# Performance work log

Hardware: AMD Instinct MI355X
Metric: run time of the kernel (lower is better)

Reference implementation:

```python
import jax, jax.numpy as jnp
import numpy as np

M_MARGIN = 0.25
GAMMA = 256.0
NEG_INF = jnp.float32(-1e30)


def setup_inputs() -> dict:
    key = jax.random.key(0)
    k1, k2 = jax.random.split(key)
    feature = jax.random.normal(k1, (8192, 128), dtype=jnp.float32)
    label = jax.random.randint(k2, (8192,), 0, 64, dtype=jnp.int64)
    return {"feature": feature, "label": label}


def reference(feature, label):
    # F.normalize: L2-normalize rows (eps=1e-12)
    norm = jnp.maximum(jnp.linalg.norm(feature, axis=1, keepdims=True), 1e-12)
    f = feature / norm
    sim = f @ f.T  # [N, N]
    N = sim.shape[0]

    same = label[:, None] == label[None, :]
    triu = jnp.triu(jnp.ones((N, N), dtype=bool), k=1)
    pos_mask = same & triu
    neg_mask = (~same) & triu

    sim_d = jax.lax.stop_gradient(sim)  # .detach() in original
    ap = jnp.maximum(-sim_d + 1.0 + M_MARGIN, 0.0)
    an = jnp.maximum(sim_d + M_MARGIN, 0.0)
    delta_p = 1.0 - M_MARGIN
    delta_n = M_MARGIN

    logit_p = -ap * (sim - delta_p) * GAMMA
    logit_n = an * (sim - delta_n) * GAMMA

    # boolean-gather + logsumexp == masked logsumexp (fixed shapes, jit-friendly)
    lse_p = jax.nn.logsumexp(jnp.where(pos_mask, logit_p, NEG_INF))
    lse_n = jax.nn.logsumexp(jnp.where(neg_mask, logit_n, NEG_INF))

    return jax.nn.softplus(lse_n + lse_p)
```

## Files before the change

### kernel.cpp

```cpp
#include <hip/hip_runtime.h>
#include <hip/hip_bf16.h>
#include <math.h>

#define NROW 8192
#define DIM  128
#define BM   64
#define BN   128
#define TM   (NROW / BM)
#define TN   (NROW / BN)
#define NTILES 4160

typedef __bf16 bf16x8 __attribute__((ext_vector_type(8)));
typedef float  f32x4  __attribute__((ext_vector_type(4)));

#define G2      369.3299304675746f
#define NEGBIG  (-3.0e38f)
#define NOFF    2000.0f

__global__ __launch_bounds__(256)
void prep_kernel(const float* __restrict__ f, __hip_bfloat16* __restrict__ fhi) {
    int row  = blockIdx.x * 4 + (threadIdx.x >> 6);
    int lane = threadIdx.x & 63;
    float2 v = ((const float2*)(f + (size_t)row * DIM))[lane];
    float ss = v.x * v.x + v.y * v.y;
    #pragma unroll
    for (int off = 32; off; off >>= 1) ss += __shfl_xor(ss, off, 64);
    float inv = 1.0f / fmaxf(sqrtf(ss), 1e-12f);
    __hip_bfloat162 hv;
    hv.x = __float2bfloat16(v.x * inv);
    hv.y = __float2bfloat16(v.y * inv);
    ((__hip_bfloat162*)(fhi + (size_t)row * DIM))[lane] = hv;
}

__device__ __forceinline__ int tstart(int tr) {
    int m = tr >> 1;
    int f = m * m - ((tr & 1) ? 0 : m);
    return 64 * tr - f;
}

__global__ __launch_bounds__(256, 4)
void sim_kernel(const __hip_bfloat16* __restrict__ fhi,
                const int* __restrict__ lab,
                float4* __restrict__ blockRes) {
    const int tid  = threadIdx.x;
    const int w    = tid >> 6;
    const int lane = tid & 63;
    const int lrow = lane & 15;
    const int lk   = lane >> 4;

    int bid = blockIdx.x;
    float sa = fmaxf(16384.f - 4.f * (float)bid, 0.f);
    int tr = 128 - (int)sqrtf(sa);
    if (tr > 127) tr = 127;
    if (tr < 0) tr = 0;
    while (tr > 0 && bid < tstart(tr)) --tr;
    while (bid >= tstart(tr + 1)) ++tr;
    const int tc = (tr >> 1) + (bid - tstart(tr));

    const int rowBase = tr * BM;
    const int colBase = tc * BN;

    __shared__ __align__(16) char smem[24 * 1024];
    __shared__ int labA[BM];
    __shared__ int labB[BN];
    __shared__ float red[4][4];

    if (tid < BM)                 labA[tid] = lab[rowBase + tid];
    else if (tid < BM + BN)       labB[tid - BM] = lab[colBase + (tid - BM)];

    f32x4 acc[4][2];
    #pragma unroll
    for (int mi = 0; mi < 4; ++mi)
        #pragma unroll
        for (int ni = 0; ni < 2; ++ni) acc[mi][ni] = (f32x4){0.f, 0.f, 0.f, 0.f};

    const int ncol0 = w * 32;

    const int rsub = lane >> 3;
    const int kbs  = 16 * ((lane & 7) ^ rsub);

    for (int kc = 0; kc < 2; ++kc) {
        #pragma unroll
        for (int t = 0; t < 6; ++t) {
            int seg = w * 6 + t;
            char* ldsb = smem + seg * 1024;
            int grow = (seg < 8) ? (rowBase + (seg & 7) * 8 + rsub)
                                 : (colBase + (seg - 8) * 8 + rsub);
            const char* g = (const char*)fhi + (size_t)grow * 256 + kc * 128 + kbs;
            __builtin_amdgcn_global_load_lds(
                (const __attribute__((address_space(1))) void*)g,
                (__attribute__((address_space(3))) void*)ldsb, 16, 0, 0);
        }
        __syncthreads();

        const char* As = smem;
        const char* Bs = smem + 8192;
        #pragma unroll
        for (int c = 0; c < 2; ++c) {
            int kb = c * 64 + lk * 16;
            bf16x8 bfr[2];
            #pragma unroll
            for (int ni = 0; ni < 2; ++ni) {
                int rb = ncol0 + ni * 16 + lrow;
                bfr[ni] = *(const bf16x8*)(Bs + rb * 128 + (kb ^ ((rb & 7) << 4)));
            }
            #pragma unroll
            for (int mi = 0; mi < 4; ++mi) {
                int ra = mi * 16 + lrow;
                bf16x8 afr = *(const bf16x8*)(As + ra * 128 + (kb ^ ((ra & 7) << 4)));
                #pragma unroll
                for (int ni = 0; ni < 2; ++ni)
                    acc[mi][ni] = __builtin_amdgcn_mfma_f32_16x16x32_bf16(afr, bfr[ni], acc[mi][ni], 0, 0, 0);
            }
        }
        __syncthreads();
    }

    const float Ppos = -2.0f * G2;
    const float Qpos = 0.9375f * G2;
    const float Qneg = -0.0625f * G2 - NOFF;
    float mall = NEGBIG, mneg = NEGBIG;
    const bool edge = (tc == (tr >> 1));

    int lbv[2];
    #pragma unroll
    for (int ni = 0; ni < 2; ++ni) lbv[ni] = labB[ncol0 + ni * 16 + lrow];

    #pragma unroll
    for (int mi = 0; mi < 4; ++mi) {
        int4 la4 = *(const int4*)&labA[mi * 16 + lk * 4];
        const int la[4] = {la4.x, la4.y, la4.z, la4.w};
        #pragma unroll
        for (int ni = 0; ni < 2; ++ni) {
            const int jg = colBase + ncol0 + ni * 16 + lrow;
            #pragma unroll
            for (int r = 0; r < 4; ++r) {
                float s = acc[mi][ni][r];
                bool pos = (la[r] == lbv[ni]);
                float P  = pos ? Ppos : 0.0f;
                float Qc = pos ? Qpos : Qneg;
                float base = fmaf(G2, s * s, fmaf(P, s, Qc));
                bool keep = pos || (s > -0.25f);
                float x = keep ? base : -NOFF;
                if (edge) {
                    int ig = rowBase + mi * 16 + lk * 4 + r;
                    x = (jg > ig) ? x : NEGBIG;
                }
                mall = fmaxf(mall, x);
                mneg = fmaxf(mneg, pos ? NEGBIG : x);
                acc[mi][ni][r] = x;
            }
        }
    }

    #pragma unroll
    for (int off = 32; off; off >>= 1) {
        mall = fmaxf(mall, __shfl_xor(mall, off, 64));
        mneg = fmaxf(mneg, __shfl_xor(mneg, off, 64));
    }
    if (lane == 0) { red[w][0] = mall; red[w][1] = mneg; }
    __syncthreads();
    const float mar = fmaxf(fmaxf(red[0][0], red[1][0]), fmaxf(red[2][0], red[3][0]));
    const float mnr = fmaxf(fmaxf(red[0][1], red[1][1]), fmaxf(red[2][1], red[3][1]));
    const float Mp  = (mar > -1000.f) ? mar : 0.f;
    const float Mn2 = (mnr > -2500.f) ? mnr : -1000.f;

    float sp = 0.f, sn = 0.f;
    #pragma unroll
    for (int mi = 0; mi < 4; ++mi)
        #pragma unroll
        for (int ni = 0; ni < 2; ++ni)
            #pragma unroll
            for (int r = 0; r < 4; ++r) {
                float x = acc[mi][ni][r];
                bool p2 = (x > -1000.f);
                float Ms = p2 ? Mp : Mn2;
                float e = __builtin_amdgcn_exp2f(x - Ms);
                float ep = p2 ? e : 0.f;
                sp += ep;
                sn += (e - ep);
            }

    #pragma unroll
    for (int off = 32; off; off >>= 1) {
        sp += __shfl_xor(sp, off, 64);
        sn += __shfl_xor(sn, off, 64);
    }
    __syncthreads();
    if (lane == 0) { red[w][2] = sp; red[w][3] = sn; }
    __syncthreads();
    if (tid == 0) {
        float Sp = red[0][2] + red[1][2] + red[2][2] + red[3][2];
        float Sn = red[0][3] + red[1][3] + red[2][3] + red[3][3];
        blockRes[bid] = make_float4(Mp, Sp, Mn2, Sn);
    }
}

__device__ __forceinline__ void merge2(float& m, float& s, float mo, float so) {
    float M = fmaxf(m, mo);
    s = s * __builtin_amdgcn_exp2f(m - M) + so * __builtin_amdgcn_exp2f(mo - M);
    m = M;
}

__global__ __launch_bounds__(256)
void finalize_kernel(const float4* __restrict__ blockRes, float* __restrict__ out) {
    __shared__ float red[4][4];
    int tid = threadIdx.x;
    float mp = NEGBIG, sp = 0.f, mn = NEGBIG, sn = 0.f;
    for (int i = tid; i < NTILES; i += 256) {
        float4 v = blockRes[i];
        merge2(mp, sp, v.x, v.y);
        merge2(mn, sn, v.z, v.w);
    }
    #pragma unroll
    for (int off = 32; off; off >>= 1) {
        float mo = __shfl_xor(mp, off, 64), so = __shfl_xor(sp, off, 64);
        merge2(mp, sp, mo, so);
        float mo2 = __shfl_xor(mn, off, 64), so2 = __shfl_xor(sn, off, 64);
        merge2(mn, sn, mo2, so2);
    }
    int wv = tid >> 6;
    if ((tid & 63) == 0) {
        red[wv][0] = mp; red[wv][1] = sp; red[wv][2] = mn; red[wv][3] = sn;
    }
    __syncthreads();
    if (tid == 0) {
        mp = red[0][0]; sp = red[0][1]; mn = red[0][2]; sn = red[0][3];
        #pragma unroll
        for (int q = 1; q < 4; ++q) {
            merge2(mp, sp, red[q][0], red[q][1]);
            merge2(mn, sn, red[q][2], red[q][3]);
        }
        const double LN2 = 0.6931471805599453;
        double lse_p = ((double)mp + log2((double)sp)) * LN2;
        double lse_n = ((double)mn + (double)NOFF + log2((double)sn)) * LN2;
        double xx = lse_p + lse_n;
        double r = (xx > 30.0) ? xx : log1p(exp(xx));
        out[0] = (float)r;
    }
}

extern "C" void kernel_launch(void* const* d_in, const int* in_sizes, int n_in,
                              void* d_out, int out_size, void* d_ws, size_t ws_size,
                              hipStream_t stream) {
    const float* f   = (const float*)d_in[0];
    const int*   lab = (const int*)d_in[1];
    float*  out      = (float*)d_out;

    __hip_bfloat16* fhi = (__hip_bfloat16*)d_ws;
    float4* blockRes    = (float4*)((char*)d_ws + 4u * 1024 * 1024);

    prep_kernel<<<NROW / 4, 256, 0, stream>>>(f, fhi);
    sim_kernel<<<NTILES, 256, 0, stream>>>(fhi, lab, blockRes);
    finalize_kernel<<<1, 256, 0, stream>>>(blockRes, out);
}
```

Before: 44.98 us.

## Drop block-level reductions, emit per-wave partials, vectorize epilogue with packed math

The main kernel now skips the cross-wave shared-memory max and sum reductions and their barriers. Each wave writes its own (max, sum) partial, giving four times as many entries, and the finalize kernel merges them with two interleaved accumulators. The edge/no-edge branch is hoisted out of the epilogue loop, the final k-loop barrier is removed, and the logit math is rewritten with 2-wide float vectors so packed FMA can be used. This trades some shared-memory syncs for more global partials, and it changes the negative-max fallback constant.

```diff
diff --git a/kernel.cpp b/kernel.cpp
--- a/kernel.cpp
+++ b/kernel.cpp
@@ -6,12 +6,12 @@
 #define DIM  128
 #define BM   64
 #define BN   128
-#define TM   (NROW / BM)
-#define TN   (NROW / BN)
 #define NTILES 4160
+#define NT4    (NTILES * 4)
 
 typedef __bf16 bf16x8 __attribute__((ext_vector_type(8)));
 typedef float  f32x4  __attribute__((ext_vector_type(4)));
+typedef float  f32x2  __attribute__((ext_vector_type(2)));
 
 #define G2      369.3299304675746f
 #define NEGBIG  (-3.0e38f)
@@ -63,10 +63,9 @@
     __shared__ __align__(16) char smem[24 * 1024];
     __shared__ int labA[BM];
     __shared__ int labB[BN];
-    __shared__ float red[4][4];
-
-    if (tid < BM)                 labA[tid] = lab[rowBase + tid];
-    else if (tid < BM + BN)       labB[tid - BM] = lab[colBase + (tid - BM)];
+
+    if (tid < BM)            labA[tid] = lab[rowBase + tid];
+    else if (tid < BM + BN)  labB[tid - BM] = lab[colBase + (tid - BM)];
 
     f32x4 acc[4][2];
     #pragma unroll
@@ -75,7 +74,6 @@
         for (int ni = 0; ni < 2; ++ni) acc[mi][ni] = (f32x4){0.f, 0.f, 0.f, 0.f};
 
     const int ncol0 = w * 32;
-
     const int rsub = lane >> 3;
     const int kbs  = 16 * ((lane & 7) ^ rsub);
 
@@ -113,87 +111,95 @@
                     acc[mi][ni] = __builtin_amdgcn_mfma_f32_16x16x32_bf16(afr, bfr[ni], acc[mi][ni], 0, 0, 0);
             }
         }
-        __syncthreads();
-    }
-
-    const float Ppos = -2.0f * G2;
-    const float Qpos = 0.9375f * G2;
-    const float Qneg = -0.0625f * G2 - NOFF;
+        if (kc == 0) __syncthreads();
+    }
+
+    const f32x2 G2v   = {G2, G2};
+    const f32x2 Pposv = {-2.0f * G2, -2.0f * G2};
+    const f32x2 Qposv = {0.9375f * G2, 0.9375f * G2};
+    const f32x2 Qnegv = {-0.0625f * G2 - NOFF, -0.0625f * G2 - NOFF};
+    const f32x2 mq    = {-0.25f, -0.25f};
     float mall = NEGBIG, mneg = NEGBIG;
-    const bool edge = (tc == (tr >> 1));
 
     int lbv[2];
     #pragma unroll
     for (int ni = 0; ni < 2; ++ni) lbv[ni] = labB[ncol0 + ni * 16 + lrow];
 
-    #pragma unroll
-    for (int mi = 0; mi < 4; ++mi) {
-        int4 la4 = *(const int4*)&labA[mi * 16 + lk * 4];
-        const int la[4] = {la4.x, la4.y, la4.z, la4.w};
-        #pragma unroll
-        for (int ni = 0; ni < 2; ++ni) {
-            const int jg = colBase + ncol0 + ni * 16 + lrow;
-            #pragma unroll
-            for (int r = 0; r < 4; ++r) {
-                float s = acc[mi][ni][r];
-                bool pos = (la[r] == lbv[ni]);
-                float P  = pos ? Ppos : 0.0f;
-                float Qc = pos ? Qpos : Qneg;
-                float base = fmaf(G2, s * s, fmaf(P, s, Qc));
-                bool keep = pos || (s > -0.25f);
-                float x = keep ? base : -NOFF;
-                if (edge) {
-                    int ig = rowBase + mi * 16 + lk * 4 + r;
-                    x = (jg > ig) ? x : NEGBIG;
-                }
-                mall = fmaxf(mall, x);
-                mneg = fmaxf(mneg, pos ? NEGBIG : x);
-                acc[mi][ni][r] = x;
-            }
-        }
-    }
+#define PASS_A(EDGEF)                                                          \
+    _Pragma("unroll")                                                          \
+    for (int mi = 0; mi < 4; ++mi) {                                           \
+        int4 la4 = *(const int4*)&labA[mi * 16 + lk * 4];                      \
+        const int la[4] = {la4.x, la4.y, la4.z, la4.w};                        \
+        _Pragma("unroll")                                                      \
+        for (int ni = 0; ni < 2; ++ni) {                                       \
+            const int lb = lbv[ni];                                            \
+            f32x4 v = acc[mi][ni];                                             \
+            f32x2 s01 = {v.x, v.y}, s23 = {v.z, v.w};                          \
+            f32x2 xp01 = __builtin_elementwise_fma(G2v, s01 * s01,             \
+                           __builtin_elementwise_fma(Pposv, s01, Qposv));      \
+            f32x2 xp23 = __builtin_elementwise_fma(G2v, s23 * s23,             \
+                           __builtin_elementwise_fma(Pposv, s23, Qposv));      \
+            f32x2 t01 = __builtin_elementwise_max(s01, mq);                    \
+            f32x2 t23 = __builtin_elementwise_max(s23, mq);                    \
+            f32x2 xn01 = __builtin_elementwise_fma(G2v, t01 * t01, Qnegv);     \
+            f32x2 xn23 = __builtin_elementwise_fma(G2v, t23 * t23, Qnegv);     \
+            const float xpv[4] = {xp01.x, xp01.y, xp23.x, xp23.y};             \
+            const float xnv[4] = {xn01.x, xn01.y, xn23.x, xn23.y};             \
+            _Pragma("unroll")                                                  \
+            for (int r = 0; r < 4; ++r) {                                      \
+                bool pos = (la[r] == lb);                                      \
+                float x = pos ? xpv[r] : xnv[r];                               \
+                if (EDGEF) {                                                   \
+                    int ig = rowBase + mi * 16 + lk * 4 + r;                   \
+                    int jg = colBase + ncol0 + ni * 16 + lrow;                 \
+                    x = (jg > ig) ? x : NEGBIG;                                \
+                }                                                              \
+                mall = fmaxf(mall, x);                                         \
+                mneg = fmaxf(mneg, pos ? NEGBIG : x);                          \
+                acc[mi][ni][r] = x;                                            \
+            }                                                                  \
+        }                                                                      \
+    }
+
+    if (tc == (tr >> 1)) { PASS_A(true) } else { PASS_A(false) }
+#undef PASS_A
 
     #pragma unroll
     for (int off = 32; off; off >>= 1) {
         mall = fmaxf(mall, __shfl_xor(mall, off, 64));
         mneg = fmaxf(mneg, __shfl_xor(mneg, off, 64));
     }
-    if (lane == 0) { red[w][0] = mall; red[w][1] = mneg; }
-    __syncthreads();
-    const float mar = fmaxf(fmaxf(red[0][0], red[1][0]), fmaxf(red[2][0], red[3][0]));
-    const float mnr = fmaxf(fmaxf(red[0][1], red[1][1]), fmaxf(red[2][1], red[3][1]));
-    const float Mp  = (mar > -1000.f) ? mar : 0.f;
-    const float Mn2 = (mnr > -2500.f) ? mnr : -1000.f;
-
-    float sp = 0.f, sn = 0.f;
+    const float Mp  = (mall > -1000.f) ? mall : 0.f;
+    const float Mn2 = (mneg > -2500.f) ? mneg : -4000.f;
+
+    const f32x2 Mpv = {Mp, Mp}, Mnv = {Mn2, Mn2};
+    f32x2 sp2 = {0.f, 0.f}, sn2 = {0.f, 0.f};
     #pragma unroll
     for (int mi = 0; mi < 4; ++mi)
         #pragma unroll
-        for (int ni = 0; ni < 2; ++ni)
+        for (int ni = 0; ni < 2; ++ni) {
+            f32x4 v = acc[mi][ni];
             #pragma unroll
-            for (int r = 0; r < 4; ++r) {
-                float x = acc[mi][ni][r];
-                bool p2 = (x > -1000.f);
-                float Ms = p2 ? Mp : Mn2;
-                float e = __builtin_amdgcn_exp2f(x - Ms);
-                float ep = p2 ? e : 0.f;
-                sp += ep;
-                sn += (e - ep);
+            for (int h = 0; h < 2; ++h) {
+                f32x2 p = h ? (f32x2){v.z, v.w} : (f32x2){v.x, v.y};
+                f32x2 dp = p - Mpv;
+                sp2 += (f32x2){__builtin_amdgcn_exp2f(dp.x),
+                               __builtin_amdgcn_exp2f(dp.y)};
+                float xm0 = (p.x > -1000.f) ? NEGBIG : p.x;
+                float xm1 = (p.y > -1000.f) ? NEGBIG : p.y;
+                f32x2 dn = (f32x2){xm0, xm1} - Mnv;
+                sn2 += (f32x2){__builtin_amdgcn_exp2f(dn.x),
+                               __builtin_amdgcn_exp2f(dn.y)};
             }
+        }
+    float sp = sp2.x + sp2.y, sn = sn2.x + sn2.y;
 
     #pragma unroll
     for (int off = 32; off; off >>= 1) {
         sp += __shfl_xor(sp, off, 64);
         sn += __shfl_xor(sn, off, 64);
     }
-    __syncthreads();
-    if (lane == 0) { red[w][2] = sp; red[w][3] = sn; }
-    __syncthreads();
-    if (tid == 0) {
-        float Sp = red[0][2] + red[1][2] + red[2][2] + red[3][2];
-        float Sn = red[0][3] + red[1][3] + red[2][3] + red[3][3];
-        blockRes[bid] = make_float4(Mp, Sp, Mn2, Sn);
-    }
+    if (lane == 0) blockRes[bid * 4 + w] = make_float4(Mp, sp, Mn2, sn);
 }
 
 __device__ __forceinline__ void merge2(float& m, float& s, float mo, float so) {
@@ -206,12 +212,22 @@
 void finalize_kernel(const float4* __restrict__ blockRes, float* __restrict__ out) {
     __shared__ float red[4][4];
     int tid = threadIdx.x;
-    float mp = NEGBIG, sp = 0.f, mn = NEGBIG, sn = 0.f;
-    for (int i = tid; i < NTILES; i += 256) {
+    float mpa[2] = {NEGBIG, NEGBIG}, spa[2] = {0.f, 0.f};
+    float mna[2] = {NEGBIG, NEGBIG}, sna[2] = {0.f, 0.f};
+    for (int i = tid; i < NT4; i += 512) {
         float4 v = blockRes[i];
-        merge2(mp, sp, v.x, v.y);
-        merge2(mn, sn, v.z, v.w);
-    }
+        merge2(mpa[0], spa[0], v.x, v.y);
+        merge2(mna[0], sna[0], v.z, v.w);
+        int j = i + 256;
+        if (j < NT4) {
+            float4 u = blockRes[j];
+            merge2(mpa[1], spa[1], u.x, u.y);
+            merge2(mna[1], sna[1], u.z, u.w);
+        }
+    }
+    float mp = mpa[0], sp = spa[0], mn = mna[0], sn = sna[0];
+    merge2(mp, sp, mpa[1], spa[1]);
+    merge2(mn, sn, mna[1], sna[1]);
     #pragma unroll
     for (int off = 32; off; off >>= 1) {
         float mo = __shfl_xor(mp, off, 64), so = __shfl_xor(sp, off, 64);
```

New measurement: 62.35 us. +38.6%, slower.
